# Kernel tuning notes

Measured on AMD Instinct MI355X. Metric: run time of the kernel, lower is better.

The kernel has to match this reference:

```python
import jax, jax.numpy as jnp
import numpy as np

C = 256
EPS = 1e-5


def setup_inputs() -> dict:
    key = jax.random.key(0)
    ks = jax.random.split(key, 10)
    B, H, W = 4, 64, 64
    x1 = jax.random.normal(ks[0], (B, C, H, W), dtype=jnp.float32)
    x2 = jax.random.normal(ks[1], (B, C, H, W), dtype=jnp.float32)
    s = 1.0 / np.sqrt(C)
    qw = jax.random.normal(ks[2], (C, C), dtype=jnp.float32) * s
    qb = jax.random.normal(ks[3], (C,), dtype=jnp.float32) * 0.01
    kw = jax.random.normal(ks[4], (C, C), dtype=jnp.float32) * s
    kb = jax.random.normal(ks[5], (C,), dtype=jnp.float32) * 0.01
    vw = jax.random.normal(ks[6], (C, C), dtype=jnp.float32) * s
    vb = jax.random.normal(ks[7], (C,), dtype=jnp.float32) * 0.01
    ln_w = jnp.ones((C,), dtype=jnp.float32)
    ln_b = jnp.zeros((C,), dtype=jnp.float32)
    return {"x1": x1, "x2": x2, "qw": qw, "qb": qb, "kw": kw, "kb": kb,
            "vw": vw, "vb": vb, "ln_w": ln_w, "ln_b": ln_b}


def _conv1x1(x, w, b):
    # 1x1 conv == per-pixel matmul over channels. x: [B,C,H,W], w: [O,C]
    return jnp.einsum('oc,bchw->bohw', w, x) + b[None, :, None, None]


def reference(x1, x2, qw, qb, kw, kb, vw, vb, ln_w, ln_b):
    q = _conv1x1(x1, qw, qb)   # [B,C,H,W]
    k = _conv1x1(x2, kw, kb)   # [B,C,H,W]
    v = _conv1x1(x2, vw, vb)   # [B,C,H,W]
    # scores: [B,H,W,I,J]; softmax over LAST axis (j) only, as in the torch code
    scores = jnp.einsum('bchw,bcij->bhwij', q, k)
    attn = jax.nn.softmax(scores, axis=-1)
    fusion = jnp.einsum('bhwij,bcij->bchw', attn, v)  # [B,C,H,W]
    # LayerNorm2d: normalize over channel dim per spatial location
    mean = jnp.mean(fusion, axis=1, keepdims=True)
    var = jnp.var(fusion, axis=1, keepdims=True)
    normed = (fusion - mean) * jax.lax.rsqrt(var + EPS)
    return normed * ln_w[None, :, None, None] + ln_b[None, :, None, None]
```

## Files before the change

kernel.cpp:

```cpp
#include <hip/hip_runtime.h>


#define CDIM 256
#define NPOS 4096
#define BATCH 4
#define EPSV 1e-5f

typedef _Float16 f16;
typedef __attribute__((ext_vector_type(8))) _Float16 f16x8;
typedef __attribute__((ext_vector_type(4))) float f32x4;
typedef __attribute__((ext_vector_type(16))) float f32x16;

#define WST       264
#define QK_STRIDE 264
#define S_STRIDE  68
#define P_STRIDE  72
#define DQ_STRIDE 72
#define FT_STRIDE 66


static __device__ __forceinline__ f16x8 cvt8(const float* __restrict__ p) {
    float4 w0 = *(const float4*)p;
    float4 w1 = *(const float4*)(p + 4);
    f16x8 r;
    r[0] = (f16)w0.x; r[1] = (f16)w0.y; r[2] = (f16)w0.z; r[3] = (f16)w0.w;
    r[4] = (f16)w1.x; r[5] = (f16)w1.y; r[6] = (f16)w1.z; r[7] = (f16)w1.w;
    return r;
}

__global__ __launch_bounds__(256, 2) void qkv_kernel(
    const float* __restrict__ x1, const float* __restrict__ x2,
    const float* __restrict__ qw, const float* __restrict__ kw,
    const float* __restrict__ vw,
    const float* __restrict__ qb, const float* __restrict__ kb,
    const float* __restrict__ vb,
    f16* __restrict__ Qg, f16* __restrict__ Kg, f16* __restrict__ Vg)
{
    __shared__ f16 Xs[64 * WST];
    __shared__ f16 Wh[64 * WST];
    __shared__ f16 Ds[64 * DQ_STRIDE];
    __shared__ float biasS[256];

    const int id = blockIdx.x;
    const int pr  = id >> 8;
    const int rem = id & 255;
    const int b   = rem >> 6;
    const int p0  = (rem & 63) << 6;
    const float* xs   = (pr == 0) ? x1 : x2;
    const float* Wp   = pr == 0 ? qw : pr == 1 ? kw : vw;
    const float* bias = pr == 0 ? qb : pr == 1 ? kb : vb;

    const int t = threadIdx.x, w = t >> 6, l = t & 63, lm = l & 31, lh = l >> 5;
    const int pt = w & 1, ot = w >> 1;

    biasS[t] = bias[t];

    {
        const int p  = t & 63;
        const int cg = (t >> 6) * 2;
        const float* src = xs + (size_t)b * CDIM * NPOS + p0 + p;
        #pragma unroll
        for (int c = cg; c < CDIM; c += 8) {
            float a0 = src[(size_t)c * NPOS];
            float a1 = src[(size_t)(c + 1) * NPOS];
            Xs[p * WST + c]     = (f16)a0;
            Xs[p * WST + c + 1] = (f16)a1;
        }
    }

    for (int q = 0; q < 4; ++q) {
        #pragma unroll
        for (int i = 0; i < 8; ++i) {
            int g = t + i * 256;
            int row = g >> 5, col = (g & 31) * 8;
            *(f16x8*)&Wh[row * WST + col] = cvt8(Wp + (size_t)(q * 64 + row) * CDIM + col);
        }
        __syncthreads();

        f32x16 accA = {}, accB = {};
        #pragma unroll
        for (int ks = 0; ks < 16; ks += 2) {
            f16x8 x0 = *(const f16x8*)&Xs[(pt * 32 + lm) * WST + ks * 16 + lh * 8];
            f16x8 w0 = *(const f16x8*)&Wh[(ot * 32 + lm) * WST + ks * 16 + lh * 8];
            f16x8 x1v = *(const f16x8*)&Xs[(pt * 32 + lm) * WST + (ks + 1) * 16 + lh * 8];
            f16x8 w1 = *(const f16x8*)&Wh[(ot * 32 + lm) * WST + (ks + 1) * 16 + lh * 8];
            if (pr < 2) {
                accA = __builtin_amdgcn_mfma_f32_32x32x16_f16(x0, w0, accA, 0, 0, 0);
                accB = __builtin_amdgcn_mfma_f32_32x32x16_f16(x1v, w1, accB, 0, 0, 0);
            } else {
                accA = __builtin_amdgcn_mfma_f32_32x32x16_f16(w0, x0, accA, 0, 0, 0);
                accB = __builtin_amdgcn_mfma_f32_32x32x16_f16(w1, x1v, accB, 0, 0, 0);
            }
        }

        if (pr < 2) {
            int o_l = ot * 32 + lm;
            float bv = biasS[q * 64 + o_l];
            #pragma unroll
            for (int r = 0; r < 16; ++r) {
                int p_l = pt * 32 + (r & 3) + 8 * (r >> 2) + 4 * lh;
                Ds[p_l * DQ_STRIDE + o_l] = (f16)(accA[r] + accB[r] + bv);
            }
        } else {
            #pragma unroll
            for (int r = 0; r < 16; ++r) {
                int o_l = ot * 32 + (r & 3) + 8 * (r >> 2) + 4 * lh;
                Ds[o_l * DQ_STRIDE + pt * 32 + lm] =
                    (f16)(accA[r] + accB[r] + biasS[q * 64 + o_l]);
            }
        }
        __syncthreads();

        #pragma unroll
        for (int j = 0; j < 2; ++j) {
            int row = (t >> 3) + j * 32;
            int cc  = (t & 7) * 8;
            f16x8 vdat = *(const f16x8*)&Ds[row * DQ_STRIDE + cc];
            if (pr < 2) {
                f16* Out = (pr == 0) ? Qg : Kg;
                *(f16x8*)(Out + ((size_t)(b * NPOS + p0 + row)) * CDIM + q * 64 + cc) = vdat;
            } else {
                *(f16x8*)(Vg + ((size_t)(b * CDIM + q * 64 + row)) * NPOS + p0 + cc) = vdat;
            }
        }
    }
}

__global__ __launch_bounds__(512, 1) void attn_kernel(
    const f16* __restrict__ Qg, const f16* __restrict__ Kg, const f16* __restrict__ Vg,
    const float* __restrict__ ln_w, const float* __restrict__ ln_b,
    float* __restrict__ out)
{
    __shared__ f16   Ks[2][64 * QK_STRIDE];
    __shared__ float Ss[2][64 * S_STRIDE];
    __shared__ f16   Ps[2][64 * P_STRIDE];
    __shared__ float lnw_s[256], lnb_s[256];
    __shared__ float redS[4 * 64], redQ[4 * 64], mu_s[64], rs_s[64];

    const int t   = threadIdx.x;
    const int b   = blockIdx.x >> 6;
    const int p0  = (blockIdx.x & 63) << 6;
    const int w   = t >> 6;
    const int g   = t >> 8;
    const int wl  = w & 3;
    const int tl  = t & 255;
    const int l   = t & 63;
    const int lm  = l & 31;
    const int lh  = l >> 5;

    if (t < 256) { lnw_s[t] = ln_w[t]; lnb_s[t] = ln_b[t]; }

    const int spt = wl & 1;
    const int skt = wl >> 1;

    f16x8 qf[16];
    {
        const f16* qptr = Qg + (size_t)(b * NPOS + p0 + spt * 32 + lm) * CDIM + lh * 8;
        #pragma unroll
        for (int ks = 0; ks < 16; ++ks) qf[ks] = *(const f16x8*)(qptr + ks * 16);
    }

    const int kr = tl >> 5, koff = (tl & 31) * 8;
    f16x8 kreg[8];
    auto issue_k = [&](int ch) {
        const int i0 = ch * 64;
        #pragma unroll
        for (int r = 0; r < 8; ++r)
            kreg[r] = *(const f16x8*)(Kg + (size_t)(b * NPOS + i0 + r * 8 + kr) * CDIM + koff);
    };
    issue_k(g);

    const f16* vbase0 = Vg + (size_t)(b * CDIM + wl * 64 + lm) * NPOS;
    const f16* vbase1 = Vg + (size_t)(b * CDIM + wl * 64 + 32 + lm) * NPOS;

    f32x16 facc[4] = {};

    for (int it = 0; it < 32; ++it) {
        const int ch = it * 2 + g;
        const int i0 = ch * 64;

        #pragma unroll
        for (int r = 0; r < 8; ++r)
            *(f16x8*)&Ks[g][(r * 8 + kr) * QK_STRIDE + koff] = kreg[r];
        __syncthreads();

        f16x8 vf0[4], vf1[4];
        #pragma unroll
        for (int ks = 0; ks < 4; ++ks) {
            vf0[ks] = *(const f16x8*)(vbase0 + i0 + ks * 16 + lh * 8);
            vf1[ks] = *(const f16x8*)(vbase1 + i0 + ks * 16 + lh * 8);
        }

        f32x16 sacc = {};
        #pragma unroll
        for (int ks = 0; ks < 16; ++ks) {
            f16x8 bb = *(const f16x8*)&Ks[g][(skt * 32 + lm) * QK_STRIDE + ks * 16 + lh * 8];
            sacc = __builtin_amdgcn_mfma_f32_32x32x16_f16(qf[ks], bb, sacc, 0, 0, 0);
        }
        #pragma unroll
        for (int r = 0; r < 16; ++r) {
            int row = (r & 3) + 8 * (r >> 2) + 4 * lh;
            Ss[g][(spt * 32 + row) * S_STRIDE + skt * 32 + lm] = sacc[r];
        }
        __syncthreads();

        {
            const int r  = tl >> 2;
            const int sg = (tl & 3) * 16;
            const float* srow = &Ss[g][r * S_STRIDE + sg];
            float v[16];
            f32x4 a0 = *(const f32x4*)(srow);
            f32x4 a1 = *(const f32x4*)(srow + 4);
            f32x4 a2 = *(const f32x4*)(srow + 8);
            f32x4 a3 = *(const f32x4*)(srow + 12);
            v[0]=a0[0]; v[1]=a0[1]; v[2]=a0[2]; v[3]=a0[3];
            v[4]=a1[0]; v[5]=a1[1]; v[6]=a1[2]; v[7]=a1[3];
            v[8]=a2[0]; v[9]=a2[1]; v[10]=a2[2]; v[11]=a2[3];
            v[12]=a3[0]; v[13]=a3[1]; v[14]=a3[2]; v[15]=a3[3];
            float m = v[0];
            #pragma unroll
            for (int i = 1; i < 16; ++i) m = fmaxf(m, v[i]);
            m = fmaxf(m, __shfl_xor(m, 1));
            m = fmaxf(m, __shfl_xor(m, 2));
            float s = 0.f;
            #pragma unroll
            for (int i = 0; i < 16; ++i) { float e = __expf(v[i] - m); v[i] = e; s += e; }
            s += __shfl_xor(s, 1);
            s += __shfl_xor(s, 2);
            float inv = __builtin_amdgcn_rcpf(s);
            f16x8 h0, h1;
            #pragma unroll
            for (int i = 0; i < 8; ++i) { h0[i] = (f16)(v[i] * inv); h1[i] = (f16)(v[i + 8] * inv); }
            *(f16x8*)&Ps[g][r * P_STRIDE + sg]     = h0;
            *(f16x8*)&Ps[g][r * P_STRIDE + sg + 8] = h1;
        }
        __syncthreads();

        if (it < 31) issue_k(ch + 2);

        #pragma unroll
        for (int ks = 0; ks < 4; ++ks) {
            f16x8 bp0 = *(const f16x8*)&Ps[g][lm * P_STRIDE + ks * 16 + lh * 8];
            f16x8 bp1 = *(const f16x8*)&Ps[g][(32 + lm) * P_STRIDE + ks * 16 + lh * 8];
            facc[0] = __builtin_amdgcn_mfma_f32_32x32x16_f16(vf0[ks], bp0, facc[0], 0, 0, 0);
            facc[1] = __builtin_amdgcn_mfma_f32_32x32x16_f16(vf0[ks], bp1, facc[1], 0, 0, 0);
            facc[2] = __builtin_amdgcn_mfma_f32_32x32x16_f16(vf1[ks], bp0, facc[2], 0, 0, 0);
            facc[3] = __builtin_amdgcn_mfma_f32_32x32x16_f16(vf1[ks], bp1, facc[3], 0, 0, 0);
        }
    }

    float* Ftmp = (float*)&Ks[0][0];
    __syncthreads();
    if (g == 1) {
        #pragma unroll
        for (int ii = 0; ii < 2; ++ii)
            #pragma unroll
            for (int jj = 0; jj < 2; ++jj)
                #pragma unroll
                for (int r = 0; r < 16; ++r) {
                    int c = wl * 64 + ii * 32 + (r & 3) + 8 * (r >> 2) + 4 * lh;
                    int p = jj * 32 + lm;
                    Ftmp[c * FT_STRIDE + p] = facc[ii * 2 + jj][r];
                }
    }
    __syncthreads();
    float ps0 = 0.f, ps1 = 0.f, pq0 = 0.f, pq1 = 0.f;
    if (g == 0) {
        #pragma unroll
        for (int ii = 0; ii < 2; ++ii)
            #pragma unroll
            for (int jj = 0; jj < 2; ++jj)
                #pragma unroll
                for (int r = 0; r < 16; ++r) {
                    int c = wl * 64 + ii * 32 + (r & 3) + 8 * (r >> 2) + 4 * lh;
                    int p = jj * 32 + lm;
                    facc[ii * 2 + jj][r] += Ftmp[c * FT_STRIDE + p];
                }
        #pragma unroll
        for (int ii = 0; ii < 2; ++ii) {
            #pragma unroll
            for (int r = 0; r < 16; ++r) {
                float a = facc[ii * 2 + 0][r];
                float c = facc[ii * 2 + 1][r];
                ps0 += a; pq0 += a * a;
                ps1 += c; pq1 += c * c;
            }
        }
        ps0 += __shfl_xor(ps0, 32); pq0 += __shfl_xor(pq0, 32);
        ps1 += __shfl_xor(ps1, 32); pq1 += __shfl_xor(pq1, 32);
        if (lh == 0) {
            redS[wl * 64 + lm] = ps0;        redQ[wl * 64 + lm] = pq0;
            redS[wl * 64 + 32 + lm] = ps1;   redQ[wl * 64 + 32 + lm] = pq1;
        }
    }
    __syncthreads();
    if (t < 64) {
        float s = redS[t] + redS[64 + t] + redS[128 + t] + redS[192 + t];
        float q = redQ[t] + redQ[64 + t] + redQ[128 + t] + redQ[192 + t];
        float mean = s * (1.0f / 256.0f);
        float var  = q * (1.0f / 256.0f) - mean * mean;
        mu_s[t] = mean;
        rs_s[t] = rsqrtf(var + EPSV);
    }
    __syncthreads();
    if (g == 0) {
        #pragma unroll
        for (int ii = 0; ii < 2; ++ii) {
            #pragma unroll
            for (int jj = 0; jj < 2; ++jj) {
                int p = jj * 32 + lm;
                float mu = mu_s[p], rs = rs_s[p];
                float* dst = out + (size_t)b * CDIM * NPOS + p0 + p;
                #pragma unroll
                for (int r = 0; r < 16; ++r) {
                    int c = wl * 64 + ii * 32 + (r & 3) + 8 * (r >> 2) + 4 * lh;
                    float vL = facc[ii * 2 + jj][r];
                    dst[(size_t)c * NPOS] = (vL - mu) * rs * lnw_s[c] + lnb_s[c];
                }
            }
        }
    }
}

extern "C" void kernel_launch(void* const* d_in, const int* in_sizes, int n_in,
                              void* d_out, int out_size, void* d_ws, size_t ws_size,
                              hipStream_t stream)
{
    const float* x1  = (const float*)d_in[0];
    const float* x2  = (const float*)d_in[1];
    const float* qw  = (const float*)d_in[2];
    const float* qb  = (const float*)d_in[3];
    const float* kw  = (const float*)d_in[4];
    const float* kb  = (const float*)d_in[5];
    const float* vw  = (const float*)d_in[6];
    const float* vb  = (const float*)d_in[7];
    const float* lnw = (const float*)d_in[8];
    const float* lnb = (const float*)d_in[9];

    const size_t tsz = (size_t)BATCH * NPOS * CDIM;
    f16* Qg  = (f16*)d_ws;
    f16* Kg  = Qg + tsz;
    f16* Vg  = Kg + tsz;

    qkv_kernel<<<768, 256, 0, stream>>>(x1, x2, qw, kw, vw, qb, kb, vb, Qg, Kg, Vg);
    attn_kernel<<<256, 512, 0, stream>>>(Qg, Kg, Vg, lnw, lnb, (float*)d_out);
}
```

Before: 230.2 us.

## Fuse QKV projection and attention into one cooperative kernel with grid sync

Merges the QKV projection kernel and the attention/LayerNorm kernel into one cooperative launch of 256 blocks of 512 threads, separated by a grid-wide sync. Each block now computes all three projections for its 64 pixels, staging x1 and x2 in a large shared buffer, instead of spreading them over 768 smaller blocks. The attention loop is also reworked to double-prefetch K chunks into registers and write the next K tile alongside the softmax, dropping one barrier per iteration. The aim is to remove the second launch and inter-kernel gap and to overlap K loads with compute. The cost is less parallelism in the projection phase (256 blocks at one per CU) and the overhead of the grid sync.

```diff
diff --git a/kernel.cpp b/kernel.cpp
--- a/kernel.cpp
+++ b/kernel.cpp
@@ -1,4 +1,7 @@
 #include <hip/hip_runtime.h>
+#include <hip/hip_cooperative_groups.h>
+
+namespace cg = cooperative_groups;
 
 
 #define CDIM 256
@@ -12,10 +15,10 @@
 typedef __attribute__((ext_vector_type(16))) float f32x16;
 
 #define WST       264
-#define QK_STRIDE 264
 #define S_STRIDE  68
 #define P_STRIDE  72
-#define DQ_STRIDE 72
+#define DS2       136
+#define DSV       72
 #define FT_STRIDE 66
 
 
@@ -28,294 +31,317 @@
     return r;
 }
 
-__global__ __launch_bounds__(256, 2) void qkv_kernel(
+__global__ __launch_bounds__(512, 1) void fused_kernel(
     const float* __restrict__ x1, const float* __restrict__ x2,
     const float* __restrict__ qw, const float* __restrict__ kw,
     const float* __restrict__ vw,
     const float* __restrict__ qb, const float* __restrict__ kb,
     const float* __restrict__ vb,
-    f16* __restrict__ Qg, f16* __restrict__ Kg, f16* __restrict__ Vg)
-{
-    __shared__ f16 Xs[64 * WST];
-    __shared__ f16 Wh[64 * WST];
-    __shared__ f16 Ds[64 * DQ_STRIDE];
-    __shared__ float biasS[256];
-
-    const int id = blockIdx.x;
-    const int pr  = id >> 8;
-    const int rem = id & 255;
-    const int b   = rem >> 6;
-    const int p0  = (rem & 63) << 6;
-    const float* xs   = (pr == 0) ? x1 : x2;
-    const float* Wp   = pr == 0 ? qw : pr == 1 ? kw : vw;
-    const float* bias = pr == 0 ? qb : pr == 1 ? kb : vb;
-
-    const int t = threadIdx.x, w = t >> 6, l = t & 63, lm = l & 31, lh = l >> 5;
-    const int pt = w & 1, ot = w >> 1;
-
-    biasS[t] = bias[t];
-
-    {
-        const int p  = t & 63;
-        const int cg = (t >> 6) * 2;
-        const float* src = xs + (size_t)b * CDIM * NPOS + p0 + p;
-        #pragma unroll
-        for (int c = cg; c < CDIM; c += 8) {
-            float a0 = src[(size_t)c * NPOS];
-            float a1 = src[(size_t)(c + 1) * NPOS];
-            Xs[p * WST + c]     = (f16)a0;
-            Xs[p * WST + c + 1] = (f16)a1;
-        }
-    }
-
-    for (int q = 0; q < 4; ++q) {
-        #pragma unroll
-        for (int i = 0; i < 8; ++i) {
-            int g = t + i * 256;
-            int row = g >> 5, col = (g & 31) * 8;
-            *(f16x8*)&Wh[row * WST + col] = cvt8(Wp + (size_t)(q * 64 + row) * CDIM + col);
-        }
-        __syncthreads();
-
-        f32x16 accA = {}, accB = {};
-        #pragma unroll
-        for (int ks = 0; ks < 16; ks += 2) {
-            f16x8 x0 = *(const f16x8*)&Xs[(pt * 32 + lm) * WST + ks * 16 + lh * 8];
-            f16x8 w0 = *(const f16x8*)&Wh[(ot * 32 + lm) * WST + ks * 16 + lh * 8];
-            f16x8 x1v = *(const f16x8*)&Xs[(pt * 32 + lm) * WST + (ks + 1) * 16 + lh * 8];
-            f16x8 w1 = *(const f16x8*)&Wh[(ot * 32 + lm) * WST + (ks + 1) * 16 + lh * 8];
-            if (pr < 2) {
-                accA = __builtin_amdgcn_mfma_f32_32x32x16_f16(x0, w0, accA, 0, 0, 0);
-                accB = __builtin_amdgcn_mfma_f32_32x32x16_f16(x1v, w1, accB, 0, 0, 0);
-            } else {
-                accA = __builtin_amdgcn_mfma_f32_32x32x16_f16(w0, x0, accA, 0, 0, 0);
-                accB = __builtin_amdgcn_mfma_f32_32x32x16_f16(w1, x1v, accB, 0, 0, 0);
-            }
-        }
-
-        if (pr < 2) {
-            int o_l = ot * 32 + lm;
-            float bv = biasS[q * 64 + o_l];
-            #pragma unroll
-            for (int r = 0; r < 16; ++r) {
-                int p_l = pt * 32 + (r & 3) + 8 * (r >> 2) + 4 * lh;
-                Ds[p_l * DQ_STRIDE + o_l] = (f16)(accA[r] + accB[r] + bv);
-            }
-        } else {
-            #pragma unroll
-            for (int r = 0; r < 16; ++r) {
-                int o_l = ot * 32 + (r & 3) + 8 * (r >> 2) + 4 * lh;
-                Ds[o_l * DQ_STRIDE + pt * 32 + lm] =
-                    (f16)(accA[r] + accB[r] + biasS[q * 64 + o_l]);
-            }
-        }
-        __syncthreads();
-
-        #pragma unroll
-        for (int j = 0; j < 2; ++j) {
-            int row = (t >> 3) + j * 32;
-            int cc  = (t & 7) * 8;
-            f16x8 vdat = *(const f16x8*)&Ds[row * DQ_STRIDE + cc];
-            if (pr < 2) {
-                f16* Out = (pr == 0) ? Qg : Kg;
-                *(f16x8*)(Out + ((size_t)(b * NPOS + p0 + row)) * CDIM + q * 64 + cc) = vdat;
-            } else {
-                *(f16x8*)(Vg + ((size_t)(b * CDIM + q * 64 + row)) * NPOS + p0 + cc) = vdat;
-            }
-        }
-    }
-}
-
-__global__ __launch_bounds__(512, 1) void attn_kernel(
-    const f16* __restrict__ Qg, const f16* __restrict__ Kg, const f16* __restrict__ Vg,
     const float* __restrict__ ln_w, const float* __restrict__ ln_b,
+    f16* __restrict__ Qg, f16* __restrict__ Kg, f16* __restrict__ Vg,
     float* __restrict__ out)
 {
-    __shared__ f16   Ks[2][64 * QK_STRIDE];
-    __shared__ float Ss[2][64 * S_STRIDE];
-    __shared__ f16   Ps[2][64 * P_STRIDE];
-    __shared__ float lnw_s[256], lnb_s[256];
-    __shared__ float redS[4 * 64], redQ[4 * 64], mu_s[64], rs_s[64];
-
-    const int t   = threadIdx.x;
-    const int b   = blockIdx.x >> 6;
-    const int p0  = (blockIdx.x & 63) << 6;
-    const int w   = t >> 6;
-    const int g   = t >> 8;
-    const int wl  = w & 3;
-    const int tl  = t & 255;
-    const int l   = t & 63;
-    const int lm  = l & 31;
-    const int lh  = l >> 5;
-
-    if (t < 256) { lnw_s[t] = ln_w[t]; lnb_s[t] = ln_b[t]; }
-
-    const int spt = wl & 1;
-    const int skt = wl >> 1;
-
-    f16x8 qf[16];
+    __shared__ __align__(16) char SM[156672];
+
+    const int t  = threadIdx.x;
+    const int b  = blockIdx.x >> 6;
+    const int p0 = (blockIdx.x & 63) << 6;
+    const int l  = t & 63, lm = l & 31, lh = l >> 5;
+
     {
-        const f16* qptr = Qg + (size_t)(b * NPOS + p0 + spt * 32 + lm) * CDIM + lh * 8;
-        #pragma unroll
-        for (int ks = 0; ks < 16; ++ks) qf[ks] = *(const f16x8*)(qptr + ks * 16);
+        f16* Xs1 = (f16*)SM;
+        f16* Xs2 = Xs1 + 64 * WST;
+        f16* Wh  = Xs2 + 64 * WST;
+        f16* Ds  = (f16*)(SM + 135168);
+        float* biasS = (float*)(SM + 153600);
+
+        const int w8 = t >> 6;
+        const int pt = w8 & 1;
+        const int oq = w8 >> 1;
+
+        if (t < 256) { biasS[t] = qb[t]; biasS[256 + t] = kb[t]; biasS[512 + t] = vb[t]; }
+
+        {
+            const int p   = t & 63;
+            const int cg2 = (t >> 6) * 2;
+            const float* s1 = x1 + (size_t)b * CDIM * NPOS + p0 + p;
+            const float* s2 = x2 + (size_t)b * CDIM * NPOS + p0 + p;
+            #pragma unroll
+            for (int c = cg2; c < CDIM; c += 16) {
+                Xs1[p * WST + c]     = (f16)s1[(size_t)c * NPOS];
+                Xs1[p * WST + c + 1] = (f16)s1[(size_t)(c + 1) * NPOS];
+                Xs2[p * WST + c]     = (f16)s2[(size_t)c * NPOS];
+                Xs2[p * WST + c + 1] = (f16)s2[(size_t)(c + 1) * NPOS];
+            }
+        }
+
+        for (int pr = 0; pr < 3; ++pr) {
+            const float* Wp = pr == 0 ? qw : pr == 1 ? kw : vw;
+            const f16* X = (pr == 0) ? Xs1 : Xs2;
+            for (int h = 0; h < 2; ++h) {
+                __syncthreads();
+                #pragma unroll
+                for (int i = 0; i < 8; ++i) {
+                    int gi = t + i * 512;
+                    int row = gi >> 5, col = (gi & 31) * 8;
+                    *(f16x8*)&Wh[row * WST + col] =
+                        cvt8(Wp + (size_t)(h * 128 + row) * CDIM + col);
+                }
+                __syncthreads();
+
+                f32x16 accA = {}, accB = {};
+                #pragma unroll
+                for (int ks = 0; ks < 16; ks += 2) {
+                    f16x8 xa = *(const f16x8*)&X[(pt * 32 + lm) * WST + ks * 16 + lh * 8];
+                    f16x8 wa = *(const f16x8*)&Wh[(oq * 32 + lm) * WST + ks * 16 + lh * 8];
+                    f16x8 xb = *(const f16x8*)&X[(pt * 32 + lm) * WST + (ks + 1) * 16 + lh * 8];
+                    f16x8 wb = *(const f16x8*)&Wh[(oq * 32 + lm) * WST + (ks + 1) * 16 + lh * 8];
+                    if (pr < 2) {
+                        accA = __builtin_amdgcn_mfma_f32_32x32x16_f16(xa, wa, accA, 0, 0, 0);
+                        accB = __builtin_amdgcn_mfma_f32_32x32x16_f16(xb, wb, accB, 0, 0, 0);
+                    } else {
+                        accA = __builtin_amdgcn_mfma_f32_32x32x16_f16(wa, xa, accA, 0, 0, 0);
+                        accB = __builtin_amdgcn_mfma_f32_32x32x16_f16(wb, xb, accB, 0, 0, 0);
+                    }
+                }
+
+                if (pr < 2) {
+                    int o_l = oq * 32 + lm;
+                    float bv = biasS[pr * 256 + h * 128 + o_l];
+                    #pragma unroll
+                    for (int r = 0; r < 16; ++r) {
+                        int p_l = pt * 32 + (r & 3) + 8 * (r >> 2) + 4 * lh;
+                        Ds[p_l * DS2 + o_l] = (f16)(accA[r] + accB[r] + bv);
+                    }
+                } else {
+                    #pragma unroll
+                    for (int r = 0; r < 16; ++r) {
+                        int o_l = oq * 32 + (r & 3) + 8 * (r >> 2) + 4 * lh;
+                        Ds[o_l * DSV + pt * 32 + lm] =
+                            (f16)(accA[r] + accB[r] + biasS[512 + h * 128 + o_l]);
+                    }
+                }
+                __syncthreads();
+
+                if (pr < 2) {
+                    f16* Out = (pr == 0) ? Qg : Kg;
+                    #pragma unroll
+                    for (int j = 0; j < 2; ++j) {
+                        int idx = t + j * 512;
+                        int row = idx >> 4;
+                        int cc  = (idx & 15) * 8;
+                        *(f16x8*)(Out + ((size_t)(b * NPOS + p0 + row)) * CDIM + h * 128 + cc) =
+                            *(const f16x8*)&Ds[row * DS2 + cc];
+                    }
+                } else {
+                    #pragma unroll
+                    for (int j = 0; j < 2; ++j) {
+                        int idx = t + j * 512;
+                        int row = idx >> 3;
+                        int cc  = (idx & 7) * 8;
+                        *(f16x8*)(Vg + ((size_t)(b * CDIM + h * 128 + row)) * NPOS + p0 + cc) =
+                            *(const f16x8*)&Ds[row * DSV + cc];
+                    }
+                }
+            }
+        }
     }
 
-    const int kr = tl >> 5, koff = (tl & 31) * 8;
-    f16x8 kreg[8];
-    auto issue_k = [&](int ch) {
-        const int i0 = ch * 64;
+    cg::this_grid().sync();
+
+    {
+        f16*   Ks    = (f16*)SM;
+        float* Ss    = (float*)(SM + 67584);
+        f16*   Ps    = (f16*)(SM + 102400);
+        float* lnw_s = (float*)(SM + 120832);
+        float* lnb_s = (float*)(SM + 121856);
+        float* redS  = (float*)(SM + 122880);
+        float* redQ  = (float*)(SM + 123904);
+        float* mu_s  = (float*)(SM + 124928);
+        float* rs_s  = (float*)(SM + 125184);
+        float* Ftmp  = (float*)SM;
+
+        const int g  = t >> 8;
+        const int tl = t & 255;
+        const int wl = (t >> 6) & 3;
+
+        if (t < 256) { lnw_s[t] = ln_w[t]; lnb_s[t] = ln_b[t]; }
+
+        const int spt = wl & 1;
+        const int skt = wl >> 1;
+
+        f16*   KsG = Ks + g * 64 * WST;
+        float* SsG = Ss + g * 64 * S_STRIDE;
+        f16*   PsG = Ps + g * 64 * P_STRIDE;
+
+        f16x8 qf[16];
+        {
+            const f16* qptr = Qg + (size_t)(b * NPOS + p0 + spt * 32 + lm) * CDIM + lh * 8;
+            #pragma unroll
+            for (int ks = 0; ks < 16; ++ks) qf[ks] = *(const f16x8*)(qptr + ks * 16);
+        }
+
+        const int kr = tl >> 5, koff = (tl & 31) * 8;
+        f16x8 kreg[8];
+        auto issue_k = [&](int ch) {
+            const int i0 = ch * 64;
+            #pragma unroll
+            for (int r = 0; r < 8; ++r)
+                kreg[r] = *(const f16x8*)(Kg + (size_t)(b * NPOS + i0 + r * 8 + kr) * CDIM + koff);
+        };
+
+        const f16* vbase0 = Vg + (size_t)(b * CDIM + wl * 64 + lm) * NPOS;
+        const f16* vbase1 = Vg + (size_t)(b * CDIM + wl * 64 + 32 + lm) * NPOS;
+
+        issue_k(g);
         #pragma unroll
         for (int r = 0; r < 8; ++r)
-            kreg[r] = *(const f16x8*)(Kg + (size_t)(b * NPOS + i0 + r * 8 + kr) * CDIM + koff);
-    };
-    issue_k(g);
-
-    const f16* vbase0 = Vg + (size_t)(b * CDIM + wl * 64 + lm) * NPOS;
-    const f16* vbase1 = Vg + (size_t)(b * CDIM + wl * 64 + 32 + lm) * NPOS;
-
-    f32x16 facc[4] = {};
-
-    for (int it = 0; it < 32; ++it) {
-        const int ch = it * 2 + g;
-        const int i0 = ch * 64;
-
-        #pragma unroll
-        for (int r = 0; r < 8; ++r)
-            *(f16x8*)&Ks[g][(r * 8 + kr) * QK_STRIDE + koff] = kreg[r];
-        __syncthreads();
-
-        f16x8 vf0[4], vf1[4];
-        #pragma unroll
-        for (int ks = 0; ks < 4; ++ks) {
-            vf0[ks] = *(const f16x8*)(vbase0 + i0 + ks * 16 + lh * 8);
-            vf1[ks] = *(const f16x8*)(vbase1 + i0 + ks * 16 + lh * 8);
-        }
-
-        f32x16 sacc = {};
-        #pragma unroll
-        for (int ks = 0; ks < 16; ++ks) {
-            f16x8 bb = *(const f16x8*)&Ks[g][(skt * 32 + lm) * QK_STRIDE + ks * 16 + lh * 8];
-            sacc = __builtin_amdgcn_mfma_f32_32x32x16_f16(qf[ks], bb, sacc, 0, 0, 0);
-        }
-        #pragma unroll
-        for (int r = 0; r < 16; ++r) {
-            int row = (r & 3) + 8 * (r >> 2) + 4 * lh;
-            Ss[g][(spt * 32 + row) * S_STRIDE + skt * 32 + lm] = sacc[r];
-        }
-        __syncthreads();
-
-        {
-            const int r  = tl >> 2;
-            const int sg = (tl & 3) * 16;
-            const float* srow = &Ss[g][r * S_STRIDE + sg];
-            float v[16];
-            f32x4 a0 = *(const f32x4*)(srow);
-            f32x4 a1 = *(const f32x4*)(srow + 4);
-            f32x4 a2 = *(const f32x4*)(srow + 8);
-            f32x4 a3 = *(const f32x4*)(srow + 12);
-            v[0]=a0[0]; v[1]=a0[1]; v[2]=a0[2]; v[3]=a0[3];
-            v[4]=a1[0]; v[5]=a1[1]; v[6]=a1[2]; v[7]=a1[3];
-            v[8]=a2[0]; v[9]=a2[1]; v[10]=a2[2]; v[11]=a2[3];
-            v[12]=a3[0]; v[13]=a3[1]; v[14]=a3[2]; v[15]=a3[3];
-            float m = v[0];
-            #pragma unroll
-            for (int i = 1; i < 16; ++i) m = fmaxf(m, v[i]);
-            m = fmaxf(m, __shfl_xor(m, 1));
-            m = fmaxf(m, __shfl_xor(m, 2));
-            float s = 0.f;
-            #pragma unroll
-            for (int i = 0; i < 16; ++i) { float e = __expf(v[i] - m); v[i] = e; s += e; }
-            s += __shfl_xor(s, 1);
-            s += __shfl_xor(s, 2);
-            float inv = __builtin_amdgcn_rcpf(s);
-            f16x8 h0, h1;
-            #pragma unroll
-            for (int i = 0; i < 8; ++i) { h0[i] = (f16)(v[i] * inv); h1[i] = (f16)(v[i + 8] * inv); }
-            *(f16x8*)&Ps[g][r * P_STRIDE + sg]     = h0;
-            *(f16x8*)&Ps[g][r * P_STRIDE + sg + 8] = h1;
-        }
-        __syncthreads();
-
-        if (it < 31) issue_k(ch + 2);
-
-        #pragma unroll
-        for (int ks = 0; ks < 4; ++ks) {
-            f16x8 bp0 = *(const f16x8*)&Ps[g][lm * P_STRIDE + ks * 16 + lh * 8];
-            f16x8 bp1 = *(const f16x8*)&Ps[g][(32 + lm) * P_STRIDE + ks * 16 + lh * 8];
-            facc[0] = __builtin_amdgcn_mfma_f32_32x32x16_f16(vf0[ks], bp0, facc[0], 0, 0, 0);
-            facc[1] = __builtin_amdgcn_mfma_f32_32x32x16_f16(vf0[ks], bp1, facc[1], 0, 0, 0);
-            facc[2] = __builtin_amdgcn_mfma_f32_32x32x16_f16(vf1[ks], bp0, facc[2], 0, 0, 0);
-            facc[3] = __builtin_amdgcn_mfma_f32_32x32x16_f16(vf1[ks], bp1, facc[3], 0, 0, 0);
-        }
-    }
-
-    float* Ftmp = (float*)&Ks[0][0];
-    __syncthreads();
-    if (g == 1) {
-        #pragma unroll
-        for (int ii = 0; ii < 2; ++ii)
-            #pragma unroll
-            for (int jj = 0; jj < 2; ++jj)
+            *(f16x8*)&KsG[(r * 8 + kr) * WST + koff] = kreg[r];
+        issue_k(g + 2);
+
+        f32x16 facc[4] = {};
+        __syncthreads();
+
+        for (int it = 0; it < 32; ++it) {
+            const int i0 = (2 * it + g) * 64;
+
+            f16x8 vf0[4], vf1[4];
+            #pragma unroll
+            for (int ks = 0; ks < 4; ++ks) {
+                vf0[ks] = *(const f16x8*)(vbase0 + i0 + ks * 16 + lh * 8);
+                vf1[ks] = *(const f16x8*)(vbase1 + i0 + ks * 16 + lh * 8);
+            }
+
+            f32x16 sacc = {};
+            #pragma unroll
+            for (int ks = 0; ks < 16; ++ks) {
+                f16x8 bb = *(const f16x8*)&KsG[(skt * 32 + lm) * WST + ks * 16 + lh * 8];
+                sacc = __builtin_amdgcn_mfma_f32_32x32x16_f16(qf[ks], bb, sacc, 0, 0, 0);
+            }
+            #pragma unroll
+            for (int r = 0; r < 16; ++r) {
+                int row = (r & 3) + 8 * (r >> 2) + 4 * lh;
+                SsG[(spt * 32 + row) * S_STRIDE + skt * 32 + lm] = sacc[r];
+            }
+            __syncthreads();
+
+            {
+                const int r  = tl >> 2;
+                const int sg = (tl & 3) * 16;
+                const float* srow = &SsG[r * S_STRIDE + sg];
+                float v[16];
+                f32x4 a0 = *(const f32x4*)(srow);
+                f32x4 a1 = *(const f32x4*)(srow + 4);
+                f32x4 a2 = *(const f32x4*)(srow + 8);
+                f32x4 a3 = *(const f32x4*)(srow + 12);
+                v[0]=a0[0]; v[1]=a0[1]; v[2]=a0[2]; v[3]=a0[3];
+                v[4]=a1[0]; v[5]=a1[1]; v[6]=a1[2]; v[7]=a1[3];
+                v[8]=a2[0]; v[9]=a2[1]; v[10]=a2[2]; v[11]=a2[3];
+                v[12]=a3[0]; v[13]=a3[1]; v[14]=a3[2]; v[15]=a3[3];
+                float m = v[0];
+                #pragma unroll
+                for (int i = 1; i < 16; ++i) m = fmaxf(m, v[i]);
+                m = fmaxf(m, __shfl_xor(m, 1));
+                m = fmaxf(m, __shfl_xor(m, 2));
+                float s = 0.f;
+                #pragma unroll
+                for (int i = 0; i < 16; ++i) { float e = __expf(v[i] - m); v[i] = e; s += e; }
+                s += __shfl_xor(s, 1);
+                s += __shfl_xor(s, 2);
+                float inv = __builtin_amdgcn_rcpf(s);
+                f16x8 h0, h1;
+                #pragma unroll
+                for (int i = 0; i < 8; ++i) { h0[i] = (f16)(v[i] * inv); h1[i] = (f16)(v[i + 8] * inv); }
+                *(f16x8*)&PsG[r * P_STRIDE + sg]     = h0;
+                *(f16x8*)&PsG[r * P_STRIDE + sg + 8] = h1;
+            }
+
+            if (it < 31) {
+                #pragma unroll
+                for (int r = 0; r < 8; ++r)
+                    *(f16x8*)&KsG[(r * 8 + kr) * WST + koff] = kreg[r];
+                if (it < 30) issue_k(2 * it + g + 4);
+            }
+            __syncthreads();
+
+            #pragma unroll
+            for (int ks = 0; ks < 4; ++ks) {
+                f16x8 bp0 = *(const f16x8*)&PsG[lm * P_STRIDE + ks * 16 + lh * 8];
+                f16x8 bp1 = *(const f16x8*)&PsG[(32 + lm) * P_STRIDE + ks * 16 + lh * 8];
+                facc[0] = __builtin_amdgcn_mfma_f32_32x32x16_f16(vf0[ks], bp0, facc[0], 0, 0, 0);
+                facc[1] = __builtin_amdgcn_mfma_f32_32x32x16_f16(vf0[ks], bp1, facc[1], 0, 0, 0);
+                facc[2] = __builtin_amdgcn_mfma_f32_32x32x16_f16(vf1[ks], bp0, facc[2], 0, 0, 0);
+                facc[3] = __builtin_amdgcn_mfma_f32_32x32x16_f16(vf1[ks], bp1, facc[3], 0, 0, 0);
+            }
+        }
+
+        __syncthreads();
+        if (g == 1) {
+            #pragma unroll
+            for (int ii = 0; ii < 2; ++ii)
+                #pragma unroll
+                for (int jj = 0; jj < 2; ++jj)
+                    #pragma unroll
+                    for (int r = 0; r < 16; ++r) {
+                        int c = wl * 64 + ii * 32 + (r & 3) + 8 * (r >> 2) + 4 * lh;
+                        int p = jj * 32 + lm;
+                        Ftmp[c * FT_STRIDE + p] = facc[ii * 2 + jj][r];
+                    }
+        }
+        __syncthreads();
+        if (g == 0) {
+            float ps0 = 0.f, ps1 = 0.f, pq0 = 0.f, pq1 = 0.f;
+            #pragma unroll
+            for (int ii = 0; ii < 2; ++ii)
+                #pragma unroll
+                for (int jj = 0; jj < 2; ++jj)
+                    #pragma unroll
+                    for (int r = 0; r < 16; ++r) {
+                        int c = wl * 64 + ii * 32 + (r & 3) + 8 * (r >> 2) + 4 * lh;
+                        int p = jj * 32 + lm;
+                        facc[ii * 2 + jj][r] += Ftmp[c * FT_STRIDE + p];
+                    }
+            #pragma unroll
+            for (int ii = 0; ii < 2; ++ii) {
                 #pragma unroll
                 for (int r = 0; r < 16; ++r) {
-                    int c = wl * 64 + ii * 32 + (r & 3) + 8 * (r >> 2) + 4 * lh;
+                    float a = facc[ii * 2 + 0][r];
+                    float c = facc[ii * 2 + 1][r];
+                    ps0 += a; pq0 += a * a;
+                    ps1 += c; pq1 += c * c;
+                }
+            }
+            ps0 += __shfl_xor(ps0, 32); pq0 += __shfl_xor(pq0, 32);
+            ps1 += __shfl_xor(ps1, 32); pq1 += __shfl_xor(pq1, 32);
+            if (lh == 0) {
+                redS[wl * 64 + lm] = ps0;        redQ[wl * 64 + lm] = pq0;
+                redS[wl * 64 + 32 + lm] = ps1;   redQ[wl * 64 + 32 + lm] = pq1;
+            }
+        }
+        __syncthreads();
+        if (t < 64) {
+            float s = redS[t] + redS[64 + t] + redS[128 + t] + redS[192 + t];
+            float q = redQ[t] + redQ[64 + t] + redQ[128 + t] + redQ[192 + t];
+            float mean = s * (1.0f / 256.0f);
+            float var  = q * (1.0f / 256.0f) - mean * mean;
+            mu_s[t] = mean;
+            rs_s[t] = rsqrtf(var + EPSV);
+        }
+        __syncthreads();
+        if (g == 0) {
+            #pragma unroll
+            for (int ii = 0; ii < 2; ++ii) {
+                #pragma unroll
+                for (int jj = 0; jj < 2; ++jj) {
                     int p = jj * 32 + lm;
-                    Ftmp[c * FT_STRIDE + p] = facc[ii * 2 + jj][r];
-                }
-    }
-    __syncthreads();
-    float ps0 = 0.f, ps1 = 0.f, pq0 = 0.f, pq1 = 0.f;
-    if (g == 0) {
-        #pragma unroll
-        for (int ii = 0; ii < 2; ++ii)
-            #pragma unroll
-            for (int jj = 0; jj < 2; ++jj)
-                #pragma unroll
-                for (int r = 0; r < 16; ++r) {
-                    int c = wl * 64 + ii * 32 + (r & 3) + 8 * (r >> 2) + 4 * lh;
-                    int p = jj * 32 + lm;
-                    facc[ii * 2 + jj][r] += Ftmp[c * FT_STRIDE + p];
-                }
-        #pragma unroll
-        for (int ii = 0; ii < 2; ++ii) {
-            #pragma unroll
-            for (int r = 0; r < 16; ++r) {
-                float a = facc[ii * 2 + 0][r];
-                float c = facc[ii * 2 + 1][r];
-                ps0 += a; pq0 += a * a;
-                ps1 += c; pq1 += c * c;
-            }
-        }
-        ps0 += __shfl_xor(ps0, 32); pq0 += __shfl_xor(pq0, 32);
-        ps1 += __shfl_xor(ps1, 32); pq1 += __shfl_xor(pq1, 32);
-        if (lh == 0) {
-            redS[wl * 64 + lm] = ps0;        redQ[wl * 64 + lm] = pq0;
-            redS[wl * 64 + 32 + lm] = ps1;   redQ[wl * 64 + 32 + lm] = pq1;
-        }
-    }
-    __syncthreads();
-    if (t < 64) {
-        float s = redS[t] + redS[64 + t] + redS[128 + t] + redS[192 + t];
-        float q = redQ[t] + redQ[64 + t] + redQ[128 + t] + redQ[192 + t];
-        float mean = s * (1.0f / 256.0f);
-        float var  = q * (1.0f / 256.0f) - mean * mean;
-        mu_s[t] = mean;
-        rs_s[t] = rsqrtf(var + EPSV);
-    }
-    __syncthreads();
-    if (g == 0) {
-        #pragma unroll
-        for (int ii = 0; ii < 2; ++ii) {
-            #pragma unroll
-            for (int jj = 0; jj < 2; ++jj) {
-                int p = jj * 32 + lm;
-                float mu = mu_s[p], rs = rs_s[p];
-                float* dst = out + (size_t)b * CDIM * NPOS + p0 + p;
-                #pragma unroll
-                for (int r = 0; r < 16; ++r) {
-                    int c = wl * 64 + ii * 32 + (r & 3) + 8 * (r >> 2) + 4 * lh;
-                    float vL = facc[ii * 2 + jj][r];
-                    dst[(size_t)c * NPOS] = (vL - mu) * rs * lnw_s[c] + lnb_s[c];
+                    float mu = mu_s[p], rs = rs_s[p];
+                    float* dst = out + (size_t)b * CDIM * NPOS + p0 + p;
+                    #pragma unroll
+                    for (int r = 0; r < 16; ++r) {
+                        int c = wl * 64 + ii * 32 + (r & 3) + 8 * (r >> 2) + 4 * lh;
+                        float vL = facc[ii * 2 + jj][r];
+                        dst[(size_t)c * NPOS] = (vL - mu) * rs * lnw_s[c] + lnb_s[c];
+                    }
                 }
             }
         }
@@ -341,7 +367,13 @@
     f16* Qg  = (f16*)d_ws;
     f16* Kg  = Qg + tsz;
     f16* Vg  = Kg + tsz;
-
-    qkv_kernel<<<768, 256, 0, stream>>>(x1, x2, qw, kw, vw, qb, kb, vb, Qg, Kg, Vg);
-    attn_kernel<<<256, 512, 0, stream>>>(Qg, Kg, Vg, lnw, lnb, (float*)d_out);
+    float* out = (float*)d_out;
+
+    void* args[] = {
+        (void*)&x1, (void*)&x2, (void*)&qw, (void*)&kw, (void*)&vw,
+        (void*)&qb, (void*)&kb, (void*)&vb, (void*)&lnw, (void*)&lnb,
+        (void*)&Qg, (void*)&Kg, (void*)&Vg, (void*)&out
+    };
+    hipLaunchCooperativeKernel((void*)fused_kernel, dim3(256), dim3(512),
+                               args, 0, stream);
 }
```

Measured after the change: 271.2 us. 17.8% more time.
